# Kernel optimization log

Hardware: AMD Instinct MI355X
Metric: run time of the kernel (lower is better)

Reference implementation:

```python
import jax, jax.numpy as jnp
import numpy as np

B, S, D, H, BLK, R = 2, 4096, 768, 12, 64, 3
NB = S // BLK  # 64 blocks
HD = D // H    # 64 head dim


def layer_norm(x, g, b, eps=1e-6):
    m = jnp.mean(x, -1, keepdims=True)
    v = jnp.mean((x - m) ** 2, -1, keepdims=True)
    return (x - m) / jnp.sqrt(v + eps) * g + b


def bigbird_attention(x, wq, bq, wk, bk, wv, bv, wo, bo, rand_attn):
    # x: [B,S,D]; rand_attn: [H, NB-2, R] int block indices
    def heads(t):
        return t.reshape(B, S, H, HD).transpose(0, 2, 1, 3)  # [B,H,S,HD]
    q = heads(x @ wq + bq)
    k = heads(x @ wk + bk)
    v = heads(x @ wv + bv)
    scale = 1.0 / jnp.sqrt(jnp.asarray(HD, x.dtype))

    qb = q.reshape(B, H, NB, BLK, HD)
    kb = k.reshape(B, H, NB, BLK, HD)
    vb = v.reshape(B, H, NB, BLK, HD)

    # --- global query blocks (first & last) attend to the full sequence ---
    qg = jnp.concatenate([qb[:, :, :1], qb[:, :, -1:]], axis=2)  # [B,H,2,BLK,HD]
    sg = jnp.einsum('bhnqd,bhkd->bhnqk', qg, k) * scale          # [B,H,2,BLK,S]
    og = jnp.einsum('bhnqk,bhkd->bhnqd', jax.nn.softmax(sg, -1), v)

    # --- middle query blocks: global(2) + window(3) + random(R) key blocks ---
    mids = jnp.arange(1, NB - 1)                                  # [NB-2]
    win = jnp.stack([mids - 1, mids, mids + 1], -1)               # [NB-2,3]
    glb = jnp.broadcast_to(jnp.array([0, NB - 1]), (NB - 2, 2))   # [NB-2,2]
    fixed = jnp.concatenate([glb, win], -1)                       # [NB-2,5]
    idx = jnp.concatenate(
        [jnp.broadcast_to(fixed, (H, NB - 2, 5)), rand_attn], -1)  # [H,NB-2,5+R]
    h_ix = jnp.arange(H)[:, None, None]
    km = kb[:, h_ix, idx].reshape(B, H, NB - 2, (5 + R) * BLK, HD)
    vm = vb[:, h_ix, idx].reshape(B, H, NB - 2, (5 + R) * BLK, HD)
    sm = jnp.einsum('bhnqd,bhnkd->bhnqk', qb[:, :, 1:-1], km) * scale
    om = jnp.einsum('bhnqk,bhnkd->bhnqd', jax.nn.softmax(sm, -1), vm)

    ob = jnp.concatenate([og[:, :, :1], om, og[:, :, 1:]], axis=2)  # [B,H,NB,BLK,HD]
    out = ob.reshape(B, H, S, HD).transpose(0, 2, 1, 3).reshape(B, S, D)
    return out @ wo + bo


def mlp(x, w1, b1, w2, b2):
    return jax.nn.gelu(x @ w1 + b1) @ w2 + b2


def setup_inputs() -> dict:
    key = jax.random.key(0)
    ks = jax.random.split(key, 8)
    s = 0.02
    return {
        'x': jax.random.normal(ks[0], (B, S, D, 2), jnp.float32),
        'ln1_g': jnp.ones((D,), jnp.float32),
        'ln1_b': jnp.zeros((D,), jnp.float32),
        'ln2_g': jnp.ones((D,), jnp.float32),
        'ln2_b': jnp.zeros((D,), jnp.float32),
        'wq': jax.random.normal(ks[1], (D, D), jnp.float32) * s,
        'bq': jnp.zeros((D,), jnp.float32),
        'wk': jax.random.normal(ks[2], (D, D), jnp.float32) * s,
        'bk': jnp.zeros((D,), jnp.float32),
        'wv': jax.random.normal(ks[3], (D, D), jnp.float32) * s,
        'bv': jnp.zeros((D,), jnp.float32),
        'wo': jax.random.normal(ks[4], (D, D), jnp.float32) * s,
        'bo': jnp.zeros((D,), jnp.float32),
        'w1': jax.random.normal(ks[5], (D, 4 * D), jnp.float32) * s,
        'b1': jnp.zeros((4 * D,), jnp.float32),
        'w2': jax.random.normal(ks[6], (4 * D, D), jnp.float32) * s,
        'b2': jnp.zeros((D,), jnp.float32),
        'rand_attn': jax.random.randint(ks[7], (H, NB - 2, R), 1, NB - 1),
    }


def reference(x, ln1_g, ln1_b, ln2_g, ln2_b, wq, bq, wk, bk, wv, bv, wo, bo,
              w1, b1, w2, b2, rand_attn):
    # x: [B,S,D,2]; chunk(2,-1): first chunk -> x2, second -> x1
    x2 = x[..., 0]
    x1 = x[..., 1]
    y2 = x2 + bigbird_attention(layer_norm(x1, ln1_g, ln1_b),
                                wq, bq, wk, bk, wv, bv, wo, bo, rand_attn)
    y1 = x1 + mlp(layer_norm(y2, ln2_g, ln2_b), w1, b1, w2, b2)
    return jnp.stack([y1, y2], axis=-1)  # cat([y1,y2], -1)
```

## Files before the change

### kernel.cpp

```cpp
#include <hip/hip_runtime.h>
#include <cstdint>
#include <cstddef>

typedef __attribute__((ext_vector_type(8))) short bfr8;
typedef __attribute__((ext_vector_type(4))) float acc4;

__device__ __forceinline__ float bf2f(short s) {
  return __uint_as_float(((unsigned)(unsigned short)s) << 16);
}
__device__ __forceinline__ short f2bf(float f) {
  unsigned u = __float_as_uint(f);
  u += 0x7fffu + ((u >> 16) & 1u);
  return (short)(u >> 16);
}
__device__ __forceinline__ float gelu_f(float x) {
  float z = 0.7978845608028654f * (x + 0.044715f * x * x * x);
  z = fminf(fmaxf(z, -12.f), 12.f);
  float e = __expf(2.f * z);
  float th = (e - 1.f) / (e + 1.f);
  return 0.5f * x * (1.f + th);
}
__device__ __forceinline__ void load_lds16(const short* g, short* l) {
  __builtin_amdgcn_global_load_lds(
      (const __attribute__((address_space(1))) void*)g,
      (__attribute__((address_space(3))) void*)l, 16, 0, 0);
}

#define BB 2
#define SS 4096
#define DD 768
#define HH 12
#define BLKSZ 64
#define NBLK 64
#define HDIM 64

__global__ __launch_bounds__(256) void prep_weights(
    const float* __restrict__ wq, const float* __restrict__ wk,
    const float* __restrict__ wv, const float* __restrict__ wo,
    const float* __restrict__ w1, const float* __restrict__ w2,
    const float* __restrict__ bq, const float* __restrict__ bk,
    const float* __restrict__ bv, float* __restrict__ bqkv,
    short* __restrict__ wqT, short* __restrict__ wkT, short* __restrict__ wvT,
    short* __restrict__ woT, short* __restrict__ w1T, short* __restrict__ w2T) {
  int id = blockIdx.x;
  if (id >= 6912) {
    int t = (id - 6912) * 256 + threadIdx.x;
    bqkv[t] = (t < 768) ? bq[t] : (t < 1536) ? bk[t - 768] : bv[t - 1536];
    return;
  }
  const float* src; short* dst; int K, N, n0, k0;
  if (id < 2304) {
    int seg = id / 576, local = id % 576;
    K = 768; N = 768;
    n0 = (local % 24) * 32; k0 = (local / 24) * 32;
    src = seg == 0 ? wq : seg == 1 ? wk : seg == 2 ? wv : wo;
    dst = seg == 0 ? wqT : seg == 1 ? wkT : seg == 2 ? wvT : woT;
  } else if (id < 4608) {
    int local = id - 2304;
    K = 768; N = 3072;
    n0 = (local % 96) * 32; k0 = (local / 96) * 32;
    src = w1; dst = w1T;
  } else {
    int local = id - 4608;
    K = 3072; N = 768;
    n0 = (local % 24) * 32; k0 = (local / 24) * 32;
    src = w2; dst = w2T;
  }
  __shared__ float tile[32][33];
  int tx = threadIdx.x & 31, ty = threadIdx.x >> 5;
#pragma unroll
  for (int i = 0; i < 4; i++) {
    int kk = ty + i * 8;
    tile[kk][tx] = src[(size_t)(k0 + kk) * N + n0 + tx];
  }
  __syncthreads();
#pragma unroll
  for (int i = 0; i < 4; i++) {
    int nn = ty + i * 8;
    dst[(size_t)(n0 + nn) * K + k0 + tx] = f2bf(tile[tx][nn]);
  }
}

__global__ __launch_bounds__(256) void transpose_bf16(
    const short* __restrict__ src, short* __restrict__ dst) {
  __shared__ short tile[32][33];
  int b = blockIdx.z;
  int s0 = blockIdx.x * 32, d0 = blockIdx.y * 32;
  int tx = threadIdx.x & 31, ty = threadIdx.x >> 5;
#pragma unroll
  for (int i = 0; i < 4; i++) {
    int ss = ty + i * 8;
    tile[ss][tx] = src[((size_t)b * SS + s0 + ss) * DD + d0 + tx];
  }
  __syncthreads();
#pragma unroll
  for (int i = 0; i < 4; i++) {
    int dd = ty + i * 8;
    dst[((size_t)b * DD + d0 + dd) * SS + s0 + tx] = tile[tx][dd];
  }
}

__global__ __launch_bounds__(256) void ln_kernel(
    const float* __restrict__ in, int stride, int off,
    const float* __restrict__ gam, const float* __restrict__ bet,
    short* __restrict__ out) {
  int row = blockIdx.x;
  int t = threadIdx.x;
  const float* base = in + (size_t)row * 768 * stride + off;
  float vals[3], s = 0.f, s2 = 0.f;
#pragma unroll
  for (int i = 0; i < 3; i++) {
    int d = t + 256 * i;
    float v = base[(size_t)d * stride];
    vals[i] = v; s += v; s2 += v * v;
  }
#pragma unroll
  for (int o = 32; o; o >>= 1) { s += __shfl_down(s, o); s2 += __shfl_down(s2, o); }
  __shared__ float red[8];
  int lane = t & 63, w = t >> 6;
  if (lane == 0) { red[w] = s; red[4 + w] = s2; }
  __syncthreads();
  s = red[0] + red[1] + red[2] + red[3];
  s2 = red[4] + red[5] + red[6] + red[7];
  float mean = s * (1.f / 768.f);
  float var = s2 * (1.f / 768.f) - mean * mean;
  float rstd = rsqrtf(var + 1e-6f);
#pragma unroll
  for (int i = 0; i < 3; i++) {
    int d = t + 256 * i;
    out[(size_t)row * 768 + d] = f2bf((vals[i] - mean) * rstd * gam[d] + bet[d]);
  }
}

template <int BM, int BN, int EPI>
__global__ __launch_bounds__(256) void gemm_lds(
    const short* __restrict__ A, const short* __restrict__ BT,
    const float* __restrict__ bias, const float* __restrict__ xres,
    const float* __restrict__ aux, void* __restrict__ outp, int M, int N, int K) {
  __shared__ alignas(16) short As[2][BM * 64];
  __shared__ alignas(16) short Bs[2][BN * 64];
  constexpr int TI = BM / 32;
  constexpr int TJ = BN / 32;
  int m0 = blockIdx.y * BM, n0 = blockIdx.x * BN;
  int t = threadIdx.x;
  int lane = t & 63, wave = t >> 6;
  int wm = (wave >> 1) * (BM / 2), wn = (wave & 1) * (BN / 2);
  int quad = lane >> 4, lc = lane & 15;
  acc4 acc[TI][TJ];
#pragma unroll
  for (int i = 0; i < TI; i++)
#pragma unroll
    for (int j = 0; j < TJ; j++) acc[i][j] = (acc4){0.f, 0.f, 0.f, 0.f};

  int lrow = lane >> 3;
  int scol = ((lane & 7) ^ lrow) * 8;
  const short* Ag = A + (size_t)(m0 + wave * (BM / 4) + lrow) * K + scol;
  const short* Bg = BT + (size_t)(n0 + wave * (BN / 4) + lrow) * K + scol;
  int aoff = wave * (BM * 16);
  int boff = wave * (BN * 16);
  int rsw = (lc & 7) << 4;

  const int nk = K >> 6;
#pragma unroll
  for (int j = 0; j < TI; j++)
    load_lds16(Ag + (size_t)(j * 8) * K, &As[0][aoff + j * 512]);
#pragma unroll
  for (int j = 0; j < TJ; j++)
    load_lds16(Bg + (size_t)(j * 8) * K, &Bs[0][boff + j * 512]);
  __syncthreads();

  for (int it = 0; it < nk; ++it) {
    int cur = it & 1, nxt = cur ^ 1;
    if (it + 1 < nk) {
      int k0 = (it + 1) << 6;
#pragma unroll
      for (int j = 0; j < TI; j++)
        load_lds16(Ag + k0 + (size_t)(j * 8) * K, &As[nxt][aoff + j * 512]);
#pragma unroll
      for (int j = 0; j < TJ; j++)
        load_lds16(Bg + k0 + (size_t)(j * 8) * K, &Bs[nxt][boff + j * 512]);
    }
    const char* Ab = (const char*)&As[cur][0];
    const char* Bb = (const char*)&Bs[cur][0];
#pragma unroll
    for (int kk = 0; kk < 2; kk++) {
      int rboff = ((kk << 6) | (quad << 4)) ^ rsw;
      bfr8 afr[TI], bfr[TJ];
#pragma unroll
      for (int i = 0; i < TI; i++)
        afr[i] = *(const bfr8*)(Ab + (wm + i * 16 + lc) * 128 + rboff);
#pragma unroll
      for (int j = 0; j < TJ; j++)
        bfr[j] = *(const bfr8*)(Bb + (wn + j * 16 + lc) * 128 + rboff);
#pragma unroll
      for (int i = 0; i < TI; i++)
#pragma unroll
        for (int j = 0; j < TJ; j++)
          acc[i][j] = __builtin_amdgcn_mfma_f32_16x16x32_bf16(afr[i], bfr[j], acc[i][j], 0, 0, 0);
    }
    __syncthreads();
  }
#pragma unroll
  for (int i = 0; i < TI; i++) {
#pragma unroll
    for (int j = 0; j < TJ; j++) {
      int col = n0 + wn + j * 16 + lc;
      float bv = bias[col];
#pragma unroll
      for (int r = 0; r < 4; r++) {
        int row = m0 + wm + i * 16 + quad * 4 + r;
        float v = acc[i][j][r] + bv;
        size_t idx = (size_t)row * N + col;
        if (EPI == 1) {
          v += xres[idx * 2];
          ((float*)outp)[idx * 2 + 1] = v;
        } else if (EPI == 2) {
          ((short*)outp)[idx] = f2bf(gelu_f(v));
        } else if (EPI == 3) {
          v += xres[idx * 2 + 1];
          ((float*)outp)[idx * 2] = v;
        } else if (EPI == 4) {
          int bufidx = col / 768;
          int colm = col - bufidx * 768;
          ((short*)outp)[(size_t)bufidx * 6291456 + (size_t)row * 768 + colm] = f2bf(v);
        } else if (EPI == 5) {
          v += xres[idx * 2];
          ((float*)outp)[idx] = v;
        } else {
          v += xres[idx * 2 + 1];
          float2 pr; pr.x = v; pr.y = aux[idx];
          ((float2*)outp)[idx] = pr;
        }
      }
    }
  }
}

__device__ __forceinline__ void attn_core(
    const short* __restrict__ qrow0, const short* __restrict__ kbase,
    const short* __restrict__ vt_h, const int* kblist, int nch, int t,
    short (*QPs)[72], short (*Ks)[72], short (*Vts)[72],
    float* m, float* l, acc4* O) {
  int lane = t & 63, w = t >> 6, quad = lane >> 4, lc = lane & 15;
#pragma unroll
  for (int c = t; c < 512; c += 256) {
    int r = c >> 3, dc = c & 7;
    *(bfr8*)&QPs[r][dc * 8] = *(const bfr8*)&qrow0[(size_t)r * DD + dc * 8];
  }
  __syncthreads();
  bfr8 aq0 = *(const bfr8*)&QPs[w * 16 + lc][quad * 8];
  bfr8 aq1 = *(const bfr8*)&QPs[w * 16 + lc][32 + quad * 8];
#pragma unroll
  for (int r = 0; r < 4; r++) { m[r] = -1e30f; l[r] = 0.f; }
#pragma unroll
  for (int dt = 0; dt < 4; dt++) O[dt] = (acc4){0.f, 0.f, 0.f, 0.f};

  for (int ch = 0; ch < nch; ch++) {
    int kb = kblist[ch];
    __syncthreads();
#pragma unroll
    for (int c = t; c < 512; c += 256) {
      int r = c >> 3, dc = c & 7;
      *(bfr8*)&Ks[r][dc * 8] = *(const bfr8*)&kbase[((size_t)kb * 64 + r) * DD + dc * 8];
      *(bfr8*)&Vts[r][dc * 8] = *(const bfr8*)&vt_h[(size_t)r * SS + kb * 64 + dc * 8];
    }
    __syncthreads();
    acc4 sacc[4];
#pragma unroll
    for (int nt = 0; nt < 4; nt++) {
      bfr8 bk0 = *(const bfr8*)&Ks[nt * 16 + lc][quad * 8];
      bfr8 bk1 = *(const bfr8*)&Ks[nt * 16 + lc][32 + quad * 8];
      acc4 z = (acc4){0.f, 0.f, 0.f, 0.f};
      z = __builtin_amdgcn_mfma_f32_16x16x32_bf16(aq0, bk0, z, 0, 0, 0);
      z = __builtin_amdgcn_mfma_f32_16x16x32_bf16(aq1, bk1, z, 0, 0, 0);
      sacc[nt] = z;
    }
#pragma unroll
    for (int r = 0; r < 4; r++) {
      float sv[4];
#pragma unroll
      for (int nt = 0; nt < 4; nt++) sv[nt] = sacc[nt][r] * 0.125f;
      float cm = fmaxf(fmaxf(sv[0], sv[1]), fmaxf(sv[2], sv[3]));
      cm = fmaxf(cm, __shfl_xor(cm, 1));
      cm = fmaxf(cm, __shfl_xor(cm, 2));
      cm = fmaxf(cm, __shfl_xor(cm, 4));
      cm = fmaxf(cm, __shfl_xor(cm, 8));
      float mn = fmaxf(m[r], cm);
      float al = __expf(m[r] - mn);
      m[r] = mn;
      float ls = 0.f;
#pragma unroll
      for (int nt = 0; nt < 4; nt++) {
        float p = __expf(sv[nt] - mn);
        ls += p;
        QPs[w * 16 + quad * 4 + r][nt * 16 + lc] = f2bf(p);
      }
      ls += __shfl_xor(ls, 1);
      ls += __shfl_xor(ls, 2);
      ls += __shfl_xor(ls, 4);
      ls += __shfl_xor(ls, 8);
      l[r] = l[r] * al + ls;
#pragma unroll
      for (int dt = 0; dt < 4; dt++) O[dt][r] *= al;
    }
    bfr8 ap0 = *(const bfr8*)&QPs[w * 16 + lc][quad * 8];
    bfr8 ap1 = *(const bfr8*)&QPs[w * 16 + lc][32 + quad * 8];
#pragma unroll
    for (int dt = 0; dt < 4; dt++) {
      bfr8 bv0 = *(const bfr8*)&Vts[dt * 16 + lc][quad * 8];
      bfr8 bv1 = *(const bfr8*)&Vts[dt * 16 + lc][32 + quad * 8];
      O[dt] = __builtin_amdgcn_mfma_f32_16x16x32_bf16(ap0, bv0, O[dt], 0, 0, 0);
      O[dt] = __builtin_amdgcn_mfma_f32_16x16x32_bf16(ap1, bv1, O[dt], 0, 0, 0);
    }
  }
}

__global__ __launch_bounds__(256) void attn_mid_mfma(
    const short* __restrict__ qbuf, const short* __restrict__ kbuf,
    const short* __restrict__ vtbuf, const int* __restrict__ rand_attn,
    short* __restrict__ ao) {
  int n = 1 + blockIdx.x;
  int h = blockIdx.y, b = blockIdx.z;
  int t = threadIdx.x, lane = t & 63, w = t >> 6, quad = lane >> 4, lc = lane & 15;
  int hoff = h * HDIM;
  size_t btok = (size_t)b * SS;
  __shared__ alignas(16) short QPs[64][72], Ks[64][72], Vts[64][72];
  int kblist[8];
  kblist[0] = 0; kblist[1] = NBLK - 1;
  kblist[2] = n - 1; kblist[3] = n; kblist[4] = n + 1;
#pragma unroll
  for (int r = 0; r < 3; r++)
    kblist[5 + r] = rand_attn[((size_t)h * 62 + (n - 1)) * 3 + r];
  float m[4], l[4]; acc4 O[4];
  attn_core(qbuf + (btok + (size_t)n * 64) * DD + hoff,
            kbuf + btok * DD + hoff,
            vtbuf + ((size_t)b * DD + hoff) * SS,
            kblist, 8, t, QPs, Ks, Vts, m, l, O);
#pragma unroll
  for (int r = 0; r < 4; r++) {
    float inv = 1.f / l[r];
    size_t tok = btok + (size_t)n * 64 + w * 16 + quad * 4 + r;
    short* op = ao + tok * DD + hoff;
#pragma unroll
    for (int dt = 0; dt < 4; dt++) op[dt * 16 + lc] = f2bf(O[dt][r] * inv);
  }
}

__global__ __launch_bounds__(256) void attn_glb_mfma(
    const short* __restrict__ qbuf, const short* __restrict__ kbuf,
    const short* __restrict__ vtbuf, float* __restrict__ part) {
  int g = blockIdx.x & 1, s = blockIdx.x >> 1;
  int h = blockIdx.y, b = blockIdx.z;
  int t = threadIdx.x, lane = t & 63, w = t >> 6, quad = lane >> 4, lc = lane & 15;
  int hoff = h * HDIM;
  size_t btok = (size_t)b * SS;
  int qblk = g ? (NBLK - 1) : 0;
  __shared__ alignas(16) short QPs[64][72], Ks[64][72], Vts[64][72];
  int kblist[8];
#pragma unroll
  for (int c = 0; c < 8; c++) kblist[c] = s * 8 + c;
  float m[4], l[4]; acc4 O[4];
  attn_core(qbuf + (btok + (size_t)qblk * 64) * DD + hoff,
            kbuf + btok * DD + hoff,
            vtbuf + ((size_t)b * DD + hoff) * SS,
            kblist, 8, t, QPs, Ks, Vts, m, l, O);
  float* pp = part + ((((size_t)b * HH + h) * 2 + g) * 8 + s) * 4224;
#pragma unroll
  for (int r = 0; r < 4; r++) {
    int row = w * 16 + quad * 4 + r;
#pragma unroll
    for (int dt = 0; dt < 4; dt++) pp[row * 64 + dt * 16 + lc] = O[dt][r];
    if (lc == 0) {
      pp[4096 + row] = m[r];
      pp[4160 + row] = l[r];
    }
  }
}

__global__ __launch_bounds__(256) void attn_combine(
    const float* __restrict__ part, short* __restrict__ ao) {
  int g = blockIdx.x, h = blockIdx.y, b = blockIdx.z;
  int t = threadIdx.x, qrow = t >> 2, sub = t & 3;
  const float* base = part + (((size_t)b * HH + h) * 2 + g) * 8 * 4224;
  float mm[8], ll[8], M = -1e30f;
#pragma unroll
  for (int s = 0; s < 8; s++) {
    mm[s] = base[s * 4224 + 4096 + qrow];
    ll[s] = base[s * 4224 + 4160 + qrow];
    M = fmaxf(M, mm[s]);
  }
  float L = 0.f, O[16];
#pragma unroll
  for (int d = 0; d < 16; d++) O[d] = 0.f;
#pragma unroll
  for (int s = 0; s < 8; s++) {
    float w = __expf(mm[s] - M);
    L += w * ll[s];
    const float* Op = base + s * 4224 + qrow * 64 + sub * 16;
#pragma unroll
    for (int d = 0; d < 16; d++) O[d] += w * Op[d];
  }
  float inv = 1.f / L;
  int qblk = g ? (NBLK - 1) : 0;
  size_t tok = (size_t)b * SS + (size_t)qblk * BLKSZ + qrow;
  short* op = ao + tok * DD + h * HDIM + sub * 16;
#pragma unroll
  for (int d = 0; d < 16; d++) op[d] = f2bf(O[d] * inv);
}

extern "C" void kernel_launch(void* const* d_in, const int* in_sizes, int n_in,
                              void* d_out, int out_size, void* d_ws, size_t ws_size,
                              hipStream_t stream) {
  (void)in_sizes; (void)n_in; (void)out_size;
  const float* x     = (const float*)d_in[0];
  const float* ln1_g = (const float*)d_in[1];
  const float* ln1_b = (const float*)d_in[2];
  const float* ln2_g = (const float*)d_in[3];
  const float* ln2_b = (const float*)d_in[4];
  const float* wq = (const float*)d_in[5];
  const float* bq = (const float*)d_in[6];
  const float* wk = (const float*)d_in[7];
  const float* bk = (const float*)d_in[8];
  const float* wv = (const float*)d_in[9];
  const float* bv = (const float*)d_in[10];
  const float* wo = (const float*)d_in[11];
  const float* bo = (const float*)d_in[12];
  const float* w1 = (const float*)d_in[13];
  const float* b1 = (const float*)d_in[14];
  const float* w2 = (const float*)d_in[15];
  const float* b2 = (const float*)d_in[16];
  const int* rand_attn = (const int*)d_in[17];
  float* out = (float*)d_out;

  short* wsb = (short*)d_ws;
  const size_t WD = 589824;
  const size_t WB = 2359296;
  const size_t ACT = 6291456;
  short* wqT = wsb;
  short* wkT = wqT + WD;
  short* wvT = wkT + WD;
  short* woT = wvT + WD;
  short* w1T = woT + WD;
  short* w2T = w1T + WB;
  short* xln = w2T + WB;
  short* qb  = xln + ACT;
  short* kb  = qb + ACT;
  short* vb  = kb + ACT;
  short* aob = vb + ACT;
  float* partp = (float*)(aob + ACT);
  float* bqkv = partp + 1622016;
  float* y2f  = bqkv + 2304;
  short* vbT = xln;
  short* h1 = xln;
  short* ln2b = aob;

  const size_t NEED = ((size_t)(y2f + ACT) - (size_t)d_ws);
  bool big = ws_size >= NEED;

  prep_weights<<<6921, 256, 0, stream>>>(wq, wk, wv, wo, w1, w2, bq, bk, bv, bqkv,
                                         wqT, wkT, wvT, woT, w1T, w2T);

  ln_kernel<<<8192, 256, 0, stream>>>(x, 2, 1, ln1_g, ln1_b, xln);

  gemm_lds<128, 128, 4><<<dim3(18, 64), 256, 0, stream>>>(
      xln, wqT, bqkv, nullptr, nullptr, qb, 8192, 2304, 768);

  transpose_bf16<<<dim3(128, 24, 2), 256, 0, stream>>>(vb, vbT);

  attn_mid_mfma<<<dim3(62, 12, 2), 256, 0, stream>>>(qb, kb, vbT, rand_attn, aob);
  attn_glb_mfma<<<dim3(16, 12, 2), 256, 0, stream>>>(qb, kb, vbT, partp);
  attn_combine<<<dim3(2, 12, 2), 256, 0, stream>>>(partp, aob);

  if (big) {
    gemm_lds<128, 128, 5><<<dim3(6, 64), 256, 0, stream>>>(
        aob, woT, bo, x, nullptr, y2f, 8192, 768, 768);
    ln_kernel<<<8192, 256, 0, stream>>>(y2f, 1, 0, ln2_g, ln2_b, ln2b);
    gemm_lds<128, 128, 2><<<dim3(24, 64), 256, 0, stream>>>(
        ln2b, w1T, b1, nullptr, nullptr, h1, 8192, 3072, 768);
    gemm_lds<128, 128, 6><<<dim3(6, 64), 256, 0, stream>>>(
        h1, w2T, b2, x, y2f, out, 8192, 768, 3072);
  } else {
    gemm_lds<128, 128, 1><<<dim3(6, 64), 256, 0, stream>>>(
        aob, woT, bo, x, nullptr, out, 8192, 768, 768);
    ln_kernel<<<8192, 256, 0, stream>>>((const float*)d_out, 2, 1, ln2_g, ln2_b, ln2b);
    gemm_lds<128, 128, 2><<<dim3(24, 64), 256, 0, stream>>>(
        ln2b, w1T, b1, nullptr, nullptr, h1, 8192, 3072, 768);
    gemm_lds<128, 128, 3><<<dim3(6, 64), 256, 0, stream>>>(
        h1, w2T, b2, x, nullptr, out, 8192, 768, 3072);
  }
}
```

Baseline: 455.4 us.

## Prefetch two K-tiles ahead in GEMM and remap blocks per XCD

The GEMM main loop now keeps two global-to-LDS tile loads in flight. It waits with an explicit vmcnt(8) instead of a full __syncthreads drain, and issues the load for tile it+2 into the buffer just consumed, after a barrier. Block indices are also remapped so that consecutive blocks on each of the 8 XCDs share M rows, with a different ordering for the long-K second MLP GEMM, to improve L2 reuse. The hand-written waitcnt depends on exactly 8 loads per wave per tile, which a static_assert enforces, and the extra barrier per iteration adds synchronisation cost.

```diff
diff --git a/kernel.cpp b/kernel.cpp
--- a/kernel.cpp
+++ b/kernel.cpp
@@ -132,7 +132,7 @@
   }
 }
 
-template <int BM, int BN, int EPI>
+template <int BM, int BN, int EPI, int SWZ>
 __global__ __launch_bounds__(256) void gemm_lds(
     const short* __restrict__ A, const short* __restrict__ BT,
     const float* __restrict__ bias, const float* __restrict__ xres,
@@ -141,7 +141,15 @@
   __shared__ alignas(16) short Bs[2][BN * 64];
   constexpr int TI = BM / 32;
   constexpr int TJ = BN / 32;
-  int m0 = blockIdx.y * BM, n0 = blockIdx.x * BN;
+  static_assert(TI + TJ == 8, "vmcnt(8) immediate assumes 8 loads/tile/wave");
+  int orig = blockIdx.x + gridDim.x * blockIdx.y;
+  int gx = gridDim.x;
+  int mchunk = gridDim.y >> 3;
+  int xcd = orig & 7, l = orig >> 3;
+  int mb, nb;
+  if (SWZ == 0) { nb = l / mchunk; mb = xcd * mchunk + (l % mchunk); }
+  else          { nb = l % gx;     mb = xcd * mchunk + (l / gx); }
+  int m0 = mb * BM, n0 = nb * BN;
   int t = threadIdx.x;
   int lane = t & 63, wave = t >> 6;
   int wm = (wave >> 1) * (BM / 2), wn = (wave & 1) * (BN / 2);
@@ -167,19 +175,21 @@
 #pragma unroll
   for (int j = 0; j < TJ; j++)
     load_lds16(Bg + (size_t)(j * 8) * K, &Bs[0][boff + j * 512]);
-  __syncthreads();
+  if (nk > 1) {
+#pragma unroll
+    for (int j = 0; j < TI; j++)
+      load_lds16(Ag + 64 + (size_t)(j * 8) * K, &As[1][aoff + j * 512]);
+#pragma unroll
+    for (int j = 0; j < TJ; j++)
+      load_lds16(Bg + 64 + (size_t)(j * 8) * K, &Bs[1][boff + j * 512]);
+  }
 
   for (int it = 0; it < nk; ++it) {
-    int cur = it & 1, nxt = cur ^ 1;
-    if (it + 1 < nk) {
-      int k0 = (it + 1) << 6;
-#pragma unroll
-      for (int j = 0; j < TI; j++)
-        load_lds16(Ag + k0 + (size_t)(j * 8) * K, &As[nxt][aoff + j * 512]);
-#pragma unroll
-      for (int j = 0; j < TJ; j++)
-        load_lds16(Bg + k0 + (size_t)(j * 8) * K, &Bs[nxt][boff + j * 512]);
-    }
+    int cur = it & 1;
+    if (it + 1 < nk) asm volatile("s_waitcnt vmcnt(8)" ::: "memory");
+    else             asm volatile("s_waitcnt vmcnt(0)" ::: "memory");
+    __builtin_amdgcn_s_barrier();
+    __builtin_amdgcn_sched_barrier(0);
     const char* Ab = (const char*)&As[cur][0];
     const char* Bb = (const char*)&Bs[cur][0];
 #pragma unroll
@@ -198,7 +208,18 @@
         for (int j = 0; j < TJ; j++)
           acc[i][j] = __builtin_amdgcn_mfma_f32_16x16x32_bf16(afr[i], bfr[j], acc[i][j], 0, 0, 0);
     }
-    __syncthreads();
+    if (it < nk - 2) {
+      __builtin_amdgcn_sched_barrier(0);
+      __builtin_amdgcn_s_barrier();
+      __builtin_amdgcn_sched_barrier(0);
+      int k0 = (it + 2) << 6;
+#pragma unroll
+      for (int j = 0; j < TI; j++)
+        load_lds16(Ag + k0 + (size_t)(j * 8) * K, &As[cur][aoff + j * 512]);
+#pragma unroll
+      for (int j = 0; j < TJ; j++)
+        load_lds16(Bg + k0 + (size_t)(j * 8) * K, &Bs[cur][boff + j * 512]);
+    }
   }
 #pragma unroll
   for (int i = 0; i < TI; i++) {
@@ -462,7 +483,7 @@
 
   ln_kernel<<<8192, 256, 0, stream>>>(x, 2, 1, ln1_g, ln1_b, xln);
 
-  gemm_lds<128, 128, 4><<<dim3(18, 64), 256, 0, stream>>>(
+  gemm_lds<128, 128, 4, 0><<<dim3(18, 64), 256, 0, stream>>>(
       xln, wqT, bqkv, nullptr, nullptr, qb, 8192, 2304, 768);
 
   transpose_bf16<<<dim3(128, 24, 2), 256, 0, stream>>>(vb, vbT);
@@ -472,20 +493,20 @@
   attn_combine<<<dim3(2, 12, 2), 256, 0, stream>>>(partp, aob);
 
   if (big) {
-    gemm_lds<128, 128, 5><<<dim3(6, 64), 256, 0, stream>>>(
+    gemm_lds<128, 128, 5, 0><<<dim3(6, 64), 256, 0, stream>>>(
         aob, woT, bo, x, nullptr, y2f, 8192, 768, 768);
     ln_kernel<<<8192, 256, 0, stream>>>(y2f, 1, 0, ln2_g, ln2_b, ln2b);
-    gemm_lds<128, 128, 2><<<dim3(24, 64), 256, 0, stream>>>(
+    gemm_lds<128, 128, 2, 0><<<dim3(24, 64), 256, 0, stream>>>(
         ln2b, w1T, b1, nullptr, nullptr, h1, 8192, 3072, 768);
-    gemm_lds<128, 128, 6><<<dim3(6, 64), 256, 0, stream>>>(
+    gemm_lds<128, 128, 6, 1><<<dim3(6, 64), 256, 0, stream>>>(
         h1, w2T, b2, x, y2f, out, 8192, 768, 3072);
   } else {
-    gemm_lds<128, 128, 1><<<dim3(6, 64), 256, 0, stream>>>(
+    gemm_lds<128, 128, 1, 0><<<dim3(6, 64), 256, 0, stream>>>(
         aob, woT, bo, x, nullptr, out, 8192, 768, 768);
     ln_kernel<<<8192, 256, 0, stream>>>((const float*)d_out, 2, 1, ln2_g, ln2_b, ln2b);
-    gemm_lds<128, 128, 2><<<dim3(24, 64), 256, 0, stream>>>(
+    gemm_lds<128, 128, 2, 0><<<dim3(24, 64), 256, 0, stream>>>(
         ln2b, w1T, b1, nullptr, nullptr, h1, 8192, 3072, 768);
-    gemm_lds<128, 128, 3><<<dim3(6, 64), 256, 0, stream>>>(
+    gemm_lds<128, 128, 3, 1><<<dim3(6, 64), 256, 0, stream>>>(
         h1, w2T, b2, x, nullptr, out, 8192, 768, 3072);
   }
 }
```

New measurement: 436.0 us. -4.3%, faster.
